# Performance work log

Measured on AMD Instinct MI355X. Metric: run time of the kernel, lower is better.

The kernel has to match this reference:

```python
import jax, jax.numpy as jnp
import numpy as np

TAU = 2.0  # self.temperature
EPS_GUMBEL = 1e-10
EPS_PPL = 1e-7


def setup_inputs() -> dict:
    key = jax.random.key(0)
    k1, k2, k3, k4, k5 = jax.random.split(key, 5)
    B, H = 65536, 512          # batch, conv_dim[-1]
    G, V, E = 2, 320, 256      # groups, codevectors per group, codevector_dim
    hidden_states = jax.random.normal(k1, (B, 1, H), dtype=jnp.float32)
    uniform_noise = jax.random.uniform(k2, (B, G, V), dtype=jnp.float32)
    embeddings = jax.random.uniform(k3, (G, V, E), dtype=jnp.float32, minval=-1.0, maxval=1.0)
    W_proj = jax.random.normal(k4, (G * V, H), dtype=jnp.float32) / np.sqrt(H)
    b_proj = jax.random.normal(k5, (G * V,), dtype=jnp.float32) * 0.01
    return {"hidden_states": hidden_states, "uniform_noise": uniform_noise,
            "embeddings": embeddings, "W_proj": W_proj, "b_proj": b_proj}


def reference(hidden_states, uniform_noise, embeddings, W_proj, b_proj):
    B = hidden_states.shape[0]
    G, V, E = embeddings.shape
    # weight_proj: (B, 1, H) -> (B, G*V) -> (B, G, V)
    x = hidden_states[:, 0, :]
    logits = (x @ W_proj.T + b_proj).reshape(B, G, V)
    # gumbel_softmax(tau=2, hard=True): straight-through hard one-hot
    g = -jnp.log(-jnp.log(uniform_noise + EPS_GUMBEL) + EPS_GUMBEL)
    y_soft = jax.nn.softmax((logits + g) / TAU, axis=-1)
    idx = jnp.argmax(y_soft, axis=-1)                              # (B, G)
    y_hard = jax.nn.one_hot(idx, V, dtype=y_soft.dtype)            # (B, G, V)
    gumbel_dist = y_hard - jax.lax.stop_gradient(y_soft) + y_soft  # ST estimator
    # perplexity over batch-marginal probabilities
    marginal = gumbel_dist.mean(axis=0)                            # (G, V)
    perplexity = jnp.exp(-jnp.sum(marginal * jnp.log(marginal + EPS_PPL), axis=-1)).sum()
    # select codevectors: (B, G, V) x (G, V, E) -> (B, G, E)
    selected = jnp.einsum('bgv,gve->bge', gumbel_dist, embeddings)
    return selected, perplexity
```

## Files before the change

### kernel.cpp

```cpp
#include <hip/hip_runtime.h>
#include <math.h>

#define H 512
#define GV 640
#define E_DIM 256
#define BM 64
#define KSTEP 32
#define NKT (H / KSTEP)

typedef _Float16 half8 __attribute__((ext_vector_type(8)));
typedef float f32x4 __attribute__((ext_vector_type(4)));

#define WS_WH 4096
#define WS_WL (4096 + 655360)
#define WS_NEED (4096 + 2 * 655360)

__global__ void prep_w(const float* __restrict__ W, _Float16* __restrict__ wh,
                       _Float16* __restrict__ wl)
{
    int t = blockIdx.x * 256 + threadIdx.x;
    int kt = t / 2560;
    int rem = t % 2560;
    int g = rem / 640;
    int col = rem - g * 640;
    int k = kt * KSTEP + g * 8;
    const float* src = W + (size_t)col * H + k;
    float4 v0 = *(const float4*)src;
    float4 v1 = *(const float4*)(src + 4);
    float vv[8] = {v0.x, v0.y, v0.z, v0.w, v1.x, v1.y, v1.z, v1.w};
    half8 hv, lv;
    #pragma unroll
    for (int i = 0; i < 8; ++i) {
        float ws_ = vv[i] * 1024.0f;
        _Float16 h = (_Float16)ws_;
        hv[i] = h;
        lv[i] = (_Float16)(ws_ - (float)h);
    }
    ((half8*)wh)[t] = hv;
    ((half8*)wl)[t] = lv;
}

__global__ __launch_bounds__(320, 4) void gemm_argmax_mfma(
    const float* __restrict__ hid,
    const float* __restrict__ noise,
    const float* __restrict__ emb,
    const float* __restrict__ bias,
    const _Float16* __restrict__ wh,
    const _Float16* __restrict__ wl,
    float* __restrict__ out,
    int* __restrict__ cnt)
{
    __shared__ __align__(16) _Float16 Xh[BM][KSTEP];
    __shared__ __align__(16) _Float16 Xl[BM][KSTEP];
    __shared__ int sel_n[BM];

    float* red_val = (float*)&Xh[0][0];
    int*   red_idx = (int*)&Xl[0][0];

    const int tid = threadIdx.x;
    const int w = tid >> 6;
    const int l = tid & 63;
    const int q = l & 15, g = l >> 4;
    const int sig = (q >> 1) & 3;
    const int sl = (g ^ sig) * 8;
    const int grp = blockIdx.x & 1;
    const int brow = (blockIdx.x >> 1) * BM;
    const int colbase = grp * 320 + w * 64 + q;

    f32x4 acc[4][4];
    #pragma unroll
    for (int mt = 0; mt < 4; ++mt)
        #pragma unroll
        for (int nt = 0; nt < 4; ++nt)
            acc[mt][nt] = (f32x4){0.f, 0.f, 0.f, 0.f};

    const half8* whv = (const half8*)wh;
    const half8* wlv = (const half8*)wl;

    for (int kt = 0; kt < NKT; ++kt) {
        __syncthreads();
        if (tid < 256) {
            int r = tid & 63, c = tid >> 6;
            const float* src = hid + (size_t)(brow + r) * H + kt * KSTEP + c * 8;
            float4 v0 = *(const float4*)src;
            float4 v1 = *(const float4*)(src + 4);
            float vv[8] = {v0.x, v0.y, v0.z, v0.w, v1.x, v1.y, v1.z, v1.w};
            half8 hv, lv;
            #pragma unroll
            for (int i = 0; i < 8; ++i) {
                float xs = vv[i] * 64.0f;
                _Float16 h = (_Float16)xs;
                hv[i] = h;
                lv[i] = (_Float16)(xs - (float)h);
            }
            int slot = c ^ ((r >> 1) & 3);
            *(half8*)&Xh[r][slot * 8] = hv;
            *(half8*)&Xl[r][slot * 8] = lv;
        }
        __syncthreads();

        half8 Ah[4], Al[4];
        #pragma unroll
        for (int mt = 0; mt < 4; ++mt) {
            int row = mt * 16 + q;
            Ah[mt] = *(const half8*)&Xh[row][sl];
            Al[mt] = *(const half8*)&Xl[row][sl];
        }

        const int gbase = (kt * 4 + g) * 640 + grp * 320 + w * 64 + q;
        #pragma unroll
        for (int nt = 0; nt < 4; ++nt) {
            half8 Bh = whv[gbase + nt * 16];
            half8 Bl = wlv[gbase + nt * 16];
            #pragma unroll
            for (int mt = 0; mt < 4; ++mt) {
                acc[mt][nt] = __builtin_amdgcn_mfma_f32_16x16x32_f16(Ah[mt], Bh, acc[mt][nt], 0, 0, 0);
                acc[mt][nt] = __builtin_amdgcn_mfma_f32_16x16x32_f16(Ah[mt], Bl, acc[mt][nt], 0, 0, 0);
                acc[mt][nt] = __builtin_amdgcn_mfma_f32_16x16x32_f16(Al[mt], Bh, acc[mt][nt], 0, 0, 0);
            }
        }
    }

    __syncthreads();

    const float C1 = 1.52587890625e-05f;
    float bcol[4];
    #pragma unroll
    for (int nt = 0; nt < 4; ++nt) bcol[nt] = bias[colbase + nt * 16];

    #pragma unroll
    for (int mt = 0; mt < 4; ++mt) {
        #pragma unroll
        for (int reg = 0; reg < 4; ++reg) {
            int r = mt * 16 + 4 * g + reg;
            float bv = -INFINITY;
            int bn = 0;
            #pragma unroll
            for (int nt = 0; nt < 4; ++nt) {
                int col = colbase + nt * 16;
                float u = noise[(size_t)(brow + r) * GV + col];
                float gum = -logf(-logf(u + 1e-10f) + 1e-10f);
                float z = acc[mt][nt][reg] * C1 + bcol[nt] + gum;
                if (z > bv) { bv = z; bn = col; }
            }
            #pragma unroll
            for (int m = 1; m < 16; m <<= 1) {
                float ov = __shfl_xor(bv, m, 64);
                int on = __shfl_xor(bn, m, 64);
                if (ov > bv || (ov == bv && on < bn)) { bv = ov; bn = on; }
            }
            if (q == 0) { red_val[r * 5 + w] = bv; red_idx[r * 5 + w] = bn; }
        }
    }
    __syncthreads();

    if (tid < 64) {
        int r = tid;
        float bv = -INFINITY;
        int bn = 0;
        #pragma unroll
        for (int ww = 0; ww < 5; ++ww) {
            float v = red_val[r * 5 + ww];
            int n = red_idx[r * 5 + ww];
            if (v > bv) { bv = v; bn = n; }
        }
        atomicAdd(&cnt[bn], 1);
        sel_n[r] = bn;
    }
    __syncthreads();

    if (tid < 256) {
        int r = tid >> 2, sub = tid & 3;
        int n = sel_n[r];
        const float4* src = (const float4*)(emb + (size_t)n * E_DIM);
        float4* dst = (float4*)(out + (size_t)(brow + r) * 512 + grp * 256);
        #pragma unroll
        for (int j = 0; j < 16; ++j)
            dst[sub + j * 4] = src[sub + j * 4];
    }
}

__global__ void ppl_kernel(const int* __restrict__ cnt, float* __restrict__ outp)
{
    const int lane = threadIdx.x;
    float total = 0.f;
    #pragma unroll
    for (int gg = 0; gg < 2; ++gg) {
        float s = 0.f;
        for (int v = lane; v < 320; v += 64) {
            float m = (float)cnt[gg * 320 + v] * (1.0f / 65536.0f);
            s += m * logf(m + 1e-7f);
        }
        #pragma unroll
        for (int msk = 1; msk <= 32; msk <<= 1) s += __shfl_xor(s, msk, 64);
        total += expf(-s);
    }
    if (lane == 0) *outp = total;
}

__global__ __launch_bounds__(512) void fused_gemm_argmax(
    const float* __restrict__ hid, const float* __restrict__ noise,
    const float* __restrict__ emb, const float* __restrict__ W,
    const float* __restrict__ bias, float* __restrict__ out, int* __restrict__ cnt)
{
    __shared__ float A_lds[16][64];
    __shared__ float B_lds[16][GV + 4];
    const int tid = threadIdx.x;
    const int tx = tid & 63, ty = tid >> 6;
    const int brow = blockIdx.x * 64;
    const int nbase = tx * 10;
    float acc[8][10];
    #pragma unroll
    for (int i = 0; i < 8; ++i)
        #pragma unroll
        for (int j = 0; j < 10; ++j) acc[i][j] = 0.f;
    for (int t = 0; t < H; t += 16) {
        if (t) __syncthreads();
        if (tid < 256) {
            int m = tid & 63, kq = tid >> 6;
            float4 v = *(const float4*)(hid + (size_t)(brow + m) * H + t + kq * 4);
            A_lds[kq * 4 + 0][m] = v.x; A_lds[kq * 4 + 1][m] = v.y;
            A_lds[kq * 4 + 2][m] = v.z; A_lds[kq * 4 + 3][m] = v.w;
        }
        #pragma unroll
        for (int s = 0; s < 5; ++s) {
            int c = tid + s * 512;
            int n = c % 640, kq = c / 640;
            float4 v = *(const float4*)(W + (size_t)n * H + t + kq * 4);
            B_lds[kq * 4 + 0][n] = v.x; B_lds[kq * 4 + 1][n] = v.y;
            B_lds[kq * 4 + 2][n] = v.z; B_lds[kq * 4 + 3][n] = v.w;
        }
        __syncthreads();
        #pragma unroll 4
        for (int kk = 0; kk < 16; ++kk) {
            float a[8], bb[10];
            #pragma unroll
            for (int i = 0; i < 8; ++i) a[i] = A_lds[kk][ty * 8 + i];
            #pragma unroll
            for (int j = 0; j < 10; ++j) bb[j] = B_lds[kk][nbase + j];
            #pragma unroll
            for (int i = 0; i < 8; ++i)
                #pragma unroll
                for (int j = 0; j < 10; ++j) acc[i][j] = fmaf(a[i], bb[j], acc[i][j]);
        }
    }
    float bs[10];
    #pragma unroll
    for (int j = 0; j < 10; ++j) bs[j] = bias[nbase + j];
    const int gg = tx >> 5, ll = tx & 31;
    #pragma unroll
    for (int i = 0; i < 8; ++i) {
        const int b = brow + ty * 8 + i;
        float best = -INFINITY; int bestn = nbase;
        #pragma unroll
        for (int j = 0; j < 10; ++j) {
            float u = noise[(size_t)b * GV + nbase + j];
            float gmb = -logf(-logf(u + 1e-10f) + 1e-10f);
            float z = acc[i][j] + bs[j] + gmb;
            if (z > best) { best = z; bestn = nbase + j; }
        }
        #pragma unroll
        for (int msk = 1; msk <= 16; msk <<= 1) {
            float oz = __shfl_xor(best, msk, 64);
            int on = __shfl_xor(bestn, msk, 64);
            if (oz > best || (oz == best && on < bestn)) { best = oz; bestn = on; }
        }
        if (ll == 0) atomicAdd(&cnt[bestn], 1);
        const float4* src = (const float4*)(emb + (size_t)bestn * E_DIM);
        float4* dst = (float4*)(out + (size_t)b * 512 + gg * 256);
        dst[ll] = src[ll];
        dst[ll + 32] = src[ll + 32];
    }
}

extern "C" void kernel_launch(void* const* d_in, const int* in_sizes, int n_in,
                              void* d_out, int out_size, void* d_ws, size_t ws_size,
                              hipStream_t stream)
{
    const float* hid   = (const float*)d_in[0];
    const float* noise = (const float*)d_in[1];
    const float* emb   = (const float*)d_in[2];
    const float* W     = (const float*)d_in[3];
    const float* bias  = (const float*)d_in[4];
    float* out = (float*)d_out;
    int* cnt = (int*)d_ws;
    const int B = in_sizes[0] / H;

    hipMemsetAsync(cnt, 0, GV * sizeof(int), stream);
    if (ws_size >= (size_t)WS_NEED) {
        _Float16* wh = (_Float16*)((char*)d_ws + WS_WH);
        _Float16* wl = (_Float16*)((char*)d_ws + WS_WL);
        prep_w<<<160, 256, 0, stream>>>(W, wh, wl);
        gemm_argmax_mfma<<<(B / BM) * 2, 320, 0, stream>>>(hid, noise, emb, bias, wh, wl, out, cnt);
    } else {
        fused_gemm_argmax<<<B / BM, 512, 0, stream>>>(hid, noise, emb, W, bias, out, cnt);
    }
    ppl_kernel<<<1, 64, 0, stream>>>(cnt, out + (size_t)B * 512);
}
```

Baseline: 315.3 us.

## Load A fragments directly from global memory, dropping LDS staging and barriers

Each wave now loads its own A-operand rows from global memory and does the fp16 hi/lo split in registers. This replaces the cooperative LDS staging, which needed two __syncthreads per K step. The goal is to remove the barrier stalls and the LDS round trip from the main loop. In exchange, every one of the 5 waves reloads and reconverts the same 64x32 hidden tile, so global/L1 traffic and VALU conversion work rise fivefold.

Result: slower. 441.6 us (+40.1%).

```diff
diff --git a/kernel.cpp b/kernel.cpp
--- a/kernel.cpp
+++ b/kernel.cpp
@@ -50,19 +50,14 @@
     float* __restrict__ out,
     int* __restrict__ cnt)
 {
-    __shared__ __align__(16) _Float16 Xh[BM][KSTEP];
-    __shared__ __align__(16) _Float16 Xl[BM][KSTEP];
-    __shared__ int sel_n[BM];
-
-    float* red_val = (float*)&Xh[0][0];
-    int*   red_idx = (int*)&Xl[0][0];
+    __shared__ float red_val[BM][5];
+    __shared__ int   red_idx[BM][5];
+    __shared__ int   sel_n[BM];
 
     const int tid = threadIdx.x;
     const int w = tid >> 6;
     const int l = tid & 63;
     const int q = l & 15, g = l >> 4;
-    const int sig = (q >> 1) & 3;
-    const int sl = (g ^ sig) * 8;
     const int grp = blockIdx.x & 1;
     const int brow = (blockIdx.x >> 1) * BM;
     const int colbase = grp * 320 + w * 64 + q;
@@ -78,13 +73,13 @@
     const half8* wlv = (const half8*)wl;
 
     for (int kt = 0; kt < NKT; ++kt) {
-        __syncthreads();
-        if (tid < 256) {
-            int r = tid & 63, c = tid >> 6;
-            const float* src = hid + (size_t)(brow + r) * H + kt * KSTEP + c * 8;
-            float4 v0 = *(const float4*)src;
-            float4 v1 = *(const float4*)(src + 4);
-            float vv[8] = {v0.x, v0.y, v0.z, v0.w, v1.x, v1.y, v1.z, v1.w};
+        half8 Ah[4], Al[4];
+        #pragma unroll
+        for (int mt = 0; mt < 4; ++mt) {
+            const float* aptr = hid + (size_t)(brow + mt * 16 + q) * H + kt * KSTEP + g * 8;
+            float4 a0 = *(const float4*)aptr;
+            float4 a1 = *(const float4*)(aptr + 4);
+            float vv[8] = {a0.x, a0.y, a0.z, a0.w, a1.x, a1.y, a1.z, a1.w};
             half8 hv, lv;
             #pragma unroll
             for (int i = 0; i < 8; ++i) {
@@ -93,18 +88,8 @@
                 hv[i] = h;
                 lv[i] = (_Float16)(xs - (float)h);
             }
-            int slot = c ^ ((r >> 1) & 3);
-            *(half8*)&Xh[r][slot * 8] = hv;
-            *(half8*)&Xl[r][slot * 8] = lv;
-        }
-        __syncthreads();
-
-        half8 Ah[4], Al[4];
-        #pragma unroll
-        for (int mt = 0; mt < 4; ++mt) {
-            int row = mt * 16 + q;
-            Ah[mt] = *(const half8*)&Xh[row][sl];
-            Al[mt] = *(const half8*)&Xl[row][sl];
+            Ah[mt] = hv;
+            Al[mt] = lv;
         }
 
         const int gbase = (kt * 4 + g) * 640 + grp * 320 + w * 64 + q;
@@ -120,8 +105,6 @@
             }
         }
     }
-
-    __syncthreads();
 
     const float C1 = 1.52587890625e-05f;
     float bcol[4];
@@ -149,7 +132,7 @@
                 int on = __shfl_xor(bn, m, 64);
                 if (ov > bv || (ov == bv && on < bn)) { bv = ov; bn = on; }
             }
-            if (q == 0) { red_val[r * 5 + w] = bv; red_idx[r * 5 + w] = bn; }
+            if (q == 0) { red_val[r][w] = bv; red_idx[r][w] = bn; }
         }
     }
     __syncthreads();
@@ -160,8 +143,8 @@
         int bn = 0;
         #pragma unroll
         for (int ww = 0; ww < 5; ++ww) {
-            float v = red_val[r * 5 + ww];
-            int n = red_idx[r * 5 + ww];
+            float v = red_val[r][ww];
+            int n = red_idx[r][ww];
             if (v > bv) { bv = v; bn = n; }
         }
         atomicAdd(&cnt[bn], 1);
```
